# Optimization experiments

Measured on AMD Instinct MI355X. Metric: run time of the kernel, lower is better.

Reference implementation:

```python
import jax, jax.numpy as jnp
import numpy as np

T, D, H, E, K = 8192, 1024, 4096, 8, 2


def setup_inputs() -> dict:
    key = jax.random.key(0)
    ks = jax.random.split(key, 6)
    s_in = 1.0 / np.sqrt(D)
    s_hid = 1.0 / np.sqrt(H)
    return {
        "hidden_states": jax.random.normal(ks[0], (T, D), dtype=jnp.float32),
        "router_w": jax.random.normal(ks[1], (D, E), dtype=jnp.float32) * s_in,
        "expert_w1": jax.random.normal(ks[2], (E, D, H), dtype=jnp.float32) * s_in,
        "expert_w2": jax.random.normal(ks[3], (E, H, D), dtype=jnp.float32) * s_hid,
        "shared_w1": jax.random.normal(ks[4], (D, H), dtype=jnp.float32) * s_in,
        "shared_w2": jax.random.normal(ks[5], (H, D), dtype=jnp.float32) * s_hid,
    }


def reference(hidden_states, router_w, expert_w1, expert_w2, shared_w1, shared_w2):
    x = hidden_states  # [T, D]
    # --- router: softmax over experts, keep top-k, renormalize ---
    probs = jax.nn.softmax(x @ router_w, axis=-1)            # [T, E]
    top_v, top_i = jax.lax.top_k(probs, K)                   # [T, K]
    top_v = top_v / jnp.sum(top_v, axis=-1, keepdims=True)
    # dense combine weights [T, E]; zero for non-selected experts
    comb = jnp.zeros((x.shape[0], E), x.dtype).at[
        jnp.arange(x.shape[0])[:, None], top_i].set(top_v)
    # --- routed experts (dense reference for grouped GEMM) ---
    h = jax.nn.silu(jnp.einsum('td,edh->eth', x, expert_w1))  # [E, T, H]
    eo = jnp.einsum('eth,ehd->etd', h, expert_w2)             # [E, T, D]
    routed = jnp.einsum('te,etd->td', comb, eo)               # [T, D]
    # --- shared expert, always active ---
    shared = jax.nn.silu(x @ shared_w1) @ shared_w2           # [T, D]
    return routed + shared
```

## Files before the change

kernel.cpp:

```cpp
#include <hip/hip_runtime.h>
#include <hip/hip_bf16.h>
#include <stdint.h>

typedef unsigned short u16;
typedef __attribute__((ext_vector_type(8))) short bf16x8;
typedef __attribute__((ext_vector_type(4))) float f32x4;

constexpr int T_ = 8192;
constexpr int D_ = 1024;
constexpr int H_ = 4096;
constexpr int E_ = 8;
constexpr int MAXROWS = 25600;
constexpr int NTILES  = 200;

__device__ __forceinline__ unsigned int f2bf_bits(float f) {
  unsigned int u = __float_as_uint(f);
  return (u + 0x7fffu + ((u >> 16) & 1u)) >> 16;
}

__device__ __forceinline__ void load_lds16(const void* g, void* s) {
  __builtin_amdgcn_global_load_lds(
      (const __attribute__((address_space(1))) unsigned int*)g,
      (__attribute__((address_space(3))) unsigned int*)s, 16, 0, 0);
}

__global__ __launch_bounds__(256) void router_kernel(
    const float* __restrict__ x, const float* __restrict__ rw,
    int* __restrict__ counts, int* __restrict__ tok2, float* __restrict__ wgt2) {
  __shared__ float rw_s[E_ * D_];
  __shared__ int c_s[E_];
  const int tid = threadIdx.x;
  if (tid < E_) c_s[tid] = 0;
  for (int f = tid; f < 2048; f += 256) {
    int d = f >> 1, p = f & 1;
    float4 v = *(const float4*)(rw + d * 8 + p * 4);
    rw_s[(p * 4 + 0) * D_ + d] = v.x;
    rw_s[(p * 4 + 1) * D_ + d] = v.y;
    rw_s[(p * 4 + 2) * D_ + d] = v.z;
    rw_s[(p * 4 + 3) * D_ + d] = v.w;
  }
  __syncthreads();
  const int wid = tid >> 6, lane = tid & 63;
  for (int ti = 0; ti < 16; ++ti) {
    const int t = blockIdx.x * 64 + wid * 16 + ti;
    const float* xr = x + (long)t * D_;
    float acc[E_] = {0.f, 0.f, 0.f, 0.f, 0.f, 0.f, 0.f, 0.f};
    for (int j = 0; j < 16; ++j) {
      const int d = lane + 64 * j;
      const float xv = xr[d];
#pragma unroll
      for (int e = 0; e < E_; ++e) acc[e] += xv * rw_s[e * D_ + d];
    }
#pragma unroll
    for (int off = 32; off >= 1; off >>= 1) {
#pragma unroll
      for (int e = 0; e < E_; ++e) acc[e] += __shfl_xor(acc[e], off, 64);
    }
    if (lane == 0) {
      int i0 = 0; float l0 = acc[0];
#pragma unroll
      for (int e = 1; e < E_; ++e) if (acc[e] > l0) { l0 = acc[e]; i0 = e; }
      int i1 = -1; float l1 = -3.4e38f;
#pragma unroll
      for (int e = 0; e < E_; ++e) if (e != i0 && acc[e] > l1) { l1 = acc[e]; i1 = e; }
      const float r = __expf(l1 - l0);
      const float inv = 1.f / (1.f + r);
      tok2[2 * t] = i0; tok2[2 * t + 1] = i1;
      wgt2[2 * t] = inv; wgt2[2 * t + 1] = r * inv;
      atomicAdd(&c_s[i0], 1); atomicAdd(&c_s[i1], 1);
    }
  }
  __syncthreads();
  if (tid < E_) atomicAdd(&counts[tid], c_s[tid]);
}

__global__ void scan_kernel(const int* __restrict__ counts, int* __restrict__ offs,
                            int* __restrict__ tile_expert, int* __restrict__ rowtok) {
  __shared__ int so[10];
  const int tid = threadIdx.x;
  if (tid == 0) {
    int o = 0;
    for (int e = 0; e < E_; ++e) { so[e] = o; o += ((counts[e] + 127) >> 7) << 7; }
    so[8] = o;
    o += T_;
    so[9] = o;
    for (int i = 0; i < 10; ++i) offs[i] = so[i];
  }
  __syncthreads();
  for (int i = tid; i < NTILES; i += 256) {
    const int row = i << 7;
    int e = 8;
    if (row < so[8]) {
      e = 7;
      for (int k = 0; k < 7; ++k) if (row < so[k + 1]) { e = k; break; }
    }
    tile_expert[i] = e;
  }
  for (int r = tid; r < MAXROWS; r += 256) rowtok[r] = 0;
}

__global__ __launch_bounds__(256) void assign_kernel(
    const int* __restrict__ tok2, const int* __restrict__ offs,
    int* __restrict__ cursors, int* __restrict__ rowtok, int* __restrict__ pos2) {
  __shared__ int lcnt[E_], lbase[E_];
  const int tid = threadIdx.x;
  if (tid < E_) lcnt[tid] = 0;
  __syncthreads();
  const int t = blockIdx.x * 256 + tid;
  const int e0 = tok2[2 * t], e1 = tok2[2 * t + 1];
  const int s0 = atomicAdd(&lcnt[e0], 1);
  const int s1 = atomicAdd(&lcnt[e1], 1);
  __syncthreads();
  if (tid < E_) lbase[tid] = offs[tid] + atomicAdd(&cursors[tid], lcnt[tid]);
  __syncthreads();
  const int p0 = lbase[e0] + s0, p1 = lbase[e1] + s1;
  rowtok[p0] = t; rowtok[p1] = t;
  pos2[2 * t] = p0; pos2[2 * t + 1] = p1;
  rowtok[offs[8] + t] = t;
}

__global__ __launch_bounds__(256) void cvt_x_kernel(const float* __restrict__ x,
                                                    u16* __restrict__ xb) {
  const long i = ((long)blockIdx.x * 256 + threadIdx.x) * 4;
  const float4 v = *(const float4*)(x + i);
  ushort4 o;
  o.x = (u16)f2bf_bits(v.x); o.y = (u16)f2bf_bits(v.y);
  o.z = (u16)f2bf_bits(v.z); o.w = (u16)f2bf_bits(v.w);
  *(ushort4*)(xb + i) = o;
}

__global__ __launch_bounds__(256) void transpose_cvt_kernel(
    const float* __restrict__ src8, const float* __restrict__ srcShared,
    u16* __restrict__ dst, int R, int C) {
  __shared__ float tile[64][65];
  const long stride = (long)R * C;
  const float* src = (blockIdx.z < 8) ? src8 + (long)blockIdx.z * stride : srcShared;
  u16* d = dst + (long)blockIdx.z * stride;
  const int tid = threadIdx.x;
  const int r0 = blockIdx.y * 64, c0 = blockIdx.x * 64;
  const int lr = tid >> 4, lc4 = tid & 15;
#pragma unroll
  for (int p = 0; p < 4; ++p) {
    const float4 v = *(const float4*)(src + (long)(r0 + lr + 16 * p) * C + c0 + lc4 * 4);
    tile[lr + 16 * p][lc4 * 4 + 0] = v.x;
    tile[lr + 16 * p][lc4 * 4 + 1] = v.y;
    tile[lr + 16 * p][lc4 * 4 + 2] = v.z;
    tile[lr + 16 * p][lc4 * 4 + 3] = v.w;
  }
  __syncthreads();
#pragma unroll
  for (int p = 0; p < 4; ++p) {
    const int rr = lr + 16 * p;
    ushort4 o;
    o.x = (u16)f2bf_bits(tile[lc4 * 4 + 0][rr]);
    o.y = (u16)f2bf_bits(tile[lc4 * 4 + 1][rr]);
    o.z = (u16)f2bf_bits(tile[lc4 * 4 + 2][rr]);
    o.w = (u16)f2bf_bits(tile[lc4 * 4 + 3][rr]);
    *(ushort4*)(d + (long)(c0 + rr) * R + r0 + lc4 * 4) = o;
  }
}

template <bool G1, int CHM>
__global__ __launch_bounds__(256) void moe_gemm(
    const u16* __restrict__ A, const u16* __restrict__ Bt, void* __restrict__ C,
    const int* __restrict__ rowtok, const int* __restrict__ tile_expert) {
  constexpr int K = G1 ? 1024 : 4096;
  constexpr int N = G1 ? 4096 : 1024;
  constexpr int NT = N / 128;
  __shared__ u16 As[128 * 32];
  __shared__ u16 Bs[128 * 32];

  const int tid = threadIdx.x;
  int mt, nt;
  {
    const int bid = blockIdx.x;
    const int cb = CHM * NT;
    const int chunk = bid / cb;
    const int mt0 = chunk * CHM;
    const int m = min(CHM, NTILES - mt0);
    const int rem = bid - chunk * cb;
    mt = mt0 + rem % m;
    nt = rem / m;
  }
  const int e = tile_expert[mt];

  const int sr = tid >> 2;
  const int sc = (tid & 3) << 3;

  long aoff0, aoff1;
  if constexpr (G1) {
    aoff0 = (long)rowtok[mt * 128 + sr] * K;
    aoff1 = (long)rowtok[mt * 128 + 64 + sr] * K;
  } else {
    aoff0 = (long)(mt * 128 + sr) * K;
    aoff1 = (long)(mt * 128 + 64 + sr) * K;
  }
  const u16* pa0 = A + aoff0 + sc;
  const u16* pa1 = A + aoff1 + sc;
  const u16* pb0 = Bt + (long)e * N * K + (long)(nt * 128 + sr) * K + sc;
  const u16* pb1 = pb0 + (long)64 * K;

  u16* sA0 = As + tid * 8;
  u16* sA1 = As + 2048 + tid * 8;
  u16* sB0 = Bs + tid * 8;
  u16* sB1 = Bs + 2048 + tid * 8;

  const int lane = tid & 63;
  const int wid = tid >> 6;
  const int wm = (wid >> 1) * 64;
  const int wn = (wid & 1) * 64;
  const int lr = lane & 15;
  const int quad = lane >> 4;

  f32x4 acc[4][4] = {};

  for (int k0 = 0; k0 < K; k0 += 32) {
    load_lds16(pa0 + k0, sA0);
    load_lds16(pa1 + k0, sA1);
    load_lds16(pb0 + k0, sB0);
    load_lds16(pb1 + k0, sB1);
    __syncthreads();
    bf16x8 af[4], bfv[4];
#pragma unroll
    for (int i = 0; i < 4; ++i)
      af[i] = *(const bf16x8*)(As + (wm + i * 16 + lr) * 32 + quad * 8);
#pragma unroll
    for (int j = 0; j < 4; ++j)
      bfv[j] = *(const bf16x8*)(Bs + (wn + j * 16 + lr) * 32 + quad * 8);
#pragma unroll
    for (int i = 0; i < 4; ++i)
#pragma unroll
      for (int j = 0; j < 4; ++j)
        acc[i][j] = __builtin_amdgcn_mfma_f32_16x16x32_bf16(af[i], bfv[j], acc[i][j], 0, 0, 0);
    __syncthreads();
  }

  const int rbase = mt * 128 + wm + quad * 4;
  if constexpr (G1) {
    u16* Hout = (u16*)C;
#pragma unroll
    for (int i = 0; i < 4; ++i) {
#pragma unroll
      for (int j = 0; j < 4; ++j) {
#pragma unroll
        for (int r = 0; r < 4; ++r) {
          float v = acc[i][j][r];
          v = v / (1.f + __expf(-v));
          unsigned int u = f2bf_bits(v);
          unsigned int other = (unsigned int)__shfl_xor((int)u, 1, 64);
          if (!(lane & 1)) {
            const unsigned int w = (u & 0xffffu) | (other << 16);
            const long row = rbase + i * 16 + r;
            const int col = nt * 128 + wn + j * 16 + lr;
            *(unsigned int*)(Hout + row * N + col) = w;
          }
        }
      }
    }
  } else {
    float* O = (float*)C;
#pragma unroll
    for (int i = 0; i < 4; ++i)
#pragma unroll
      for (int j = 0; j < 4; ++j)
#pragma unroll
        for (int r = 0; r < 4; ++r) {
          const long row = rbase + i * 16 + r;
          const int col = nt * 128 + wn + j * 16 + lr;
          O[row * N + col] = acc[i][j][r];
        }
  }
}

__global__ __launch_bounds__(256) void combine_kernel(
    const float* __restrict__ eo, const int* __restrict__ pos2,
    const float* __restrict__ wgt2, const int* __restrict__ offs,
    float* __restrict__ out) {
  const int t = blockIdx.x, tid = threadIdx.x;
  const int p0 = pos2[2 * t], p1 = pos2[2 * t + 1];
  const float w0 = wgt2[2 * t], w1 = wgt2[2 * t + 1];
  const int ps = offs[8] + t;
  const long c = (long)tid * 4;
  const float4 a = *(const float4*)(eo + (long)p0 * D_ + c);
  const float4 b = *(const float4*)(eo + (long)p1 * D_ + c);
  const float4 s = *(const float4*)(eo + (long)ps * D_ + c);
  float4 o;
  o.x = w0 * a.x + w1 * b.x + s.x;
  o.y = w0 * a.y + w1 * b.y + s.y;
  o.z = w0 * a.z + w1 * b.z + s.z;
  o.w = w0 * a.w + w1 * b.w + s.w;
  *(float4*)(out + (long)t * D_ + c) = o;
}

extern "C" void kernel_launch(void* const* d_in, const int* in_sizes, int n_in,
                              void* d_out, int out_size, void* d_ws, size_t ws_size,
                              hipStream_t stream) {
  const float* x   = (const float*)d_in[0];
  const float* rw  = (const float*)d_in[1];
  const float* w1  = (const float*)d_in[2];
  const float* w2  = (const float*)d_in[3];
  const float* sw1 = (const float*)d_in[4];
  const float* sw2 = (const float*)d_in[5];
  float* out = (float*)d_out;

  char* ws = (char*)d_ws;
  int*   counts      = (int*)(ws + 0);
  int*   cursors     = (int*)(ws + 64);
  int*   offs        = (int*)(ws + 128);
  int*   tile_expert = (int*)(ws + 192);
  int*   tok2        = (int*)(ws + 4096);
  float* wgt2        = (float*)(ws + 4096 + 65536);
  int*   pos2        = (int*)(ws + 4096 + 131072);
  int*   rowtok      = (int*)(ws + 4096 + 196608);

  size_t off = 1u << 20;
  u16* xb  = (u16*)(ws + off); off += (size_t)T_ * D_ * 2;
  u16* w1t = (u16*)(ws + off); off += (size_t)9 * H_ * D_ * 2;
  u16* w2t = (u16*)(ws + off); off += (size_t)9 * D_ * H_ * 2;
  u16* h   = (u16*)(ws + off); off += (size_t)MAXROWS * H_ * 2;
  float* eo = (float*)(ws + off); off += (size_t)MAXROWS * D_ * 4;

  hipMemsetAsync(ws, 0, 256, stream);
  router_kernel<<<128, 256, 0, stream>>>(x, rw, counts, tok2, wgt2);
  scan_kernel<<<1, 256, 0, stream>>>(counts, offs, tile_expert, rowtok);
  assign_kernel<<<32, 256, 0, stream>>>(tok2, offs, cursors, rowtok, pos2);
  cvt_x_kernel<<<T_ * D_ / 1024, 256, 0, stream>>>(x, xb);
  transpose_cvt_kernel<<<dim3(H_ / 64, D_ / 64, 9), 256, 0, stream>>>(w1, sw1, w1t, D_, H_);
  transpose_cvt_kernel<<<dim3(D_ / 64, H_ / 64, 9), 256, 0, stream>>>(w2, sw2, w2t, H_, D_);
  moe_gemm<true, 24><<<NTILES * (H_ / 128), 256, 0, stream>>>(xb, w1t, h, rowtok, tile_expert);
  moe_gemm<false, 64><<<NTILES * (D_ / 128), 256, 0, stream>>>(h, w2t, eo, rowtok, tile_expert);
  combine_kernel<<<T_, 256, 0, stream>>>(eo, pos2, wgt2, offs, out);
}
```

Baseline: 1.144 ms.

## Double-buffer LDS tiles in MoE GEMM to overlap loads with MFMA

```diff
diff --git a/kernel.cpp b/kernel.cpp
--- a/kernel.cpp
+++ b/kernel.cpp
@@ -167,8 +167,8 @@
   constexpr int K = G1 ? 1024 : 4096;
   constexpr int N = G1 ? 4096 : 1024;
   constexpr int NT = N / 128;
-  __shared__ u16 As[128 * 32];
-  __shared__ u16 Bs[128 * 32];
+  __shared__ u16 As[2 * 4096];
+  __shared__ u16 Bs[2 * 4096];
 
   const int tid = threadIdx.x;
   int mt, nt;
@@ -200,10 +200,10 @@
   const u16* pb0 = Bt + (long)e * N * K + (long)(nt * 128 + sr) * K + sc;
   const u16* pb1 = pb0 + (long)64 * K;
 
-  u16* sA0 = As + tid * 8;
-  u16* sA1 = As + 2048 + tid * 8;
-  u16* sB0 = Bs + tid * 8;
-  u16* sB1 = Bs + 2048 + tid * 8;
+  u16* sA0[2] = {As + tid * 8, As + 4096 + tid * 8};
+  u16* sA1[2] = {As + 2048 + tid * 8, As + 4096 + 2048 + tid * 8};
+  u16* sB0[2] = {Bs + tid * 8, Bs + 4096 + tid * 8};
+  u16* sB1[2] = {Bs + 2048 + tid * 8, Bs + 4096 + 2048 + tid * 8};
 
   const int lane = tid & 63;
   const int wid = tid >> 6;
@@ -214,25 +214,55 @@
 
   f32x4 acc[4][4] = {};
 
-  for (int k0 = 0; k0 < K; k0 += 32) {
-    load_lds16(pa0 + k0, sA0);
-    load_lds16(pa1 + k0, sA1);
-    load_lds16(pb0 + k0, sB0);
-    load_lds16(pb1 + k0, sB1);
+  load_lds16(pa0, sA0[0]);
+  load_lds16(pa1, sA1[0]);
+  load_lds16(pb0, sB0[0]);
+  load_lds16(pb1, sB1[0]);
+
+#pragma unroll 1
+  for (int k0 = 0; k0 < K; k0 += 64) {
     __syncthreads();
-    bf16x8 af[4], bfv[4];
-#pragma unroll
-    for (int i = 0; i < 4; ++i)
-      af[i] = *(const bf16x8*)(As + (wm + i * 16 + lr) * 32 + quad * 8);
-#pragma unroll
-    for (int j = 0; j < 4; ++j)
-      bfv[j] = *(const bf16x8*)(Bs + (wn + j * 16 + lr) * 32 + quad * 8);
-#pragma unroll
-    for (int i = 0; i < 4; ++i)
+    if (k0 + 32 < K) {
+      load_lds16(pa0 + k0 + 32, sA0[1]);
+      load_lds16(pa1 + k0 + 32, sA1[1]);
+      load_lds16(pb0 + k0 + 32, sB0[1]);
+      load_lds16(pb1 + k0 + 32, sB1[1]);
+    }
+    {
+      bf16x8 af[4], bfv[4];
+#pragma unroll
+      for (int i = 0; i < 4; ++i)
+        af[i] = *(const bf16x8*)(As + (wm + i * 16 + lr) * 32 + quad * 8);
 #pragma unroll
       for (int j = 0; j < 4; ++j)
-        acc[i][j] = __builtin_amdgcn_mfma_f32_16x16x32_bf16(af[i], bfv[j], acc[i][j], 0, 0, 0);
+        bfv[j] = *(const bf16x8*)(Bs + (wn + j * 16 + lr) * 32 + quad * 8);
+#pragma unroll
+      for (int i = 0; i < 4; ++i)
+#pragma unroll
+        for (int j = 0; j < 4; ++j)
+          acc[i][j] = __builtin_amdgcn_mfma_f32_16x16x32_bf16(af[i], bfv[j], acc[i][j], 0, 0, 0);
+    }
     __syncthreads();
+    if (k0 + 64 < K) {
+      load_lds16(pa0 + k0 + 64, sA0[0]);
+      load_lds16(pa1 + k0 + 64, sA1[0]);
+      load_lds16(pb0 + k0 + 64, sB0[0]);
+      load_lds16(pb1 + k0 + 64, sB1[0]);
+    }
+    {
+      bf16x8 af[4], bfv[4];
+#pragma unroll
+      for (int i = 0; i < 4; ++i)
+        af[i] = *(const bf16x8*)(As + 4096 + (wm + i * 16 + lr) * 32 + quad * 8);
+#pragma unroll
+      for (int j = 0; j < 4; ++j)
+        bfv[j] = *(const bf16x8*)(Bs + 4096 + (wn + j * 16 + lr) * 32 + quad * 8);
+#pragma unroll
+      for (int i = 0; i < 4; ++i)
+#pragma unroll
+        for (int j = 0; j < 4; ++j)
+          acc[i][j] = __builtin_amdgcn_mfma_f32_16x16x32_bf16(af[i], bfv[j], acc[i][j], 0, 0, 0);
+    }
   }
 
   const int rbase = mt * 128 + wm + quad * 4;
```

Result: faster. 1.092 ms (-4.5%).
